# Kernel tuning notes

Hardware: AMD Instinct MI355X
Metric: run time of the kernel (lower is better)

The kernel has to match this reference:

```python
import jax, jax.numpy as jnp
import numpy as np

B, SQ, SK, H, HEADS, E, DFF = 4, 512, 1024, 1024, 16, 8, 4096
DH = H // HEADS
EPS = 1e-6


def _ln(x, g, b):
    m = jnp.mean(x, -1, keepdims=True)
    v = jnp.mean((x - m) ** 2, -1, keepdims=True)
    return (x - m) * jax.lax.rsqrt(v + EPS) * g + b


def setup_inputs() -> dict:
    key = jax.random.key(0)
    ks = jax.random.split(key, 16)
    s = 0.02
    return {
        "concated_input": jax.random.normal(ks[0], (B, SK, H), jnp.float32),
        "gen_emb": jax.random.normal(ks[1], (B, SQ, H), jnp.float32),
        "mask": jnp.zeros((B, 1, SQ, SK), jnp.float32),
        "ln_g": jnp.ones((H,), jnp.float32),
        "ln_b": jnp.zeros((H,), jnp.float32),
        "wq": jax.random.normal(ks[2], (H, H), jnp.float32) * s,
        "bq": jnp.zeros((H,), jnp.float32),
        "wk": jax.random.normal(ks[3], (H, H), jnp.float32) * s,
        "bk": jnp.zeros((H,), jnp.float32),
        "wv": jax.random.normal(ks[4], (H, H), jnp.float32) * s,
        "bv": jnp.zeros((H,), jnp.float32),
        "wo": jax.random.normal(ks[5], (H, H), jnp.float32) * s,
        "bo": jnp.zeros((H,), jnp.float32),
        "gw": jax.random.normal(ks[6], (H, E), jnp.float32) * s,
        "gb": jnp.zeros((E,), jnp.float32),
        "w1": jax.random.normal(ks[7], (E, H, DFF), jnp.float32) * s,
        "b1": jnp.zeros((E, DFF), jnp.float32),
        "w2": jax.random.normal(ks[8], (E, DFF, H), jnp.float32) * s,
        "b2": jnp.zeros((E, H), jnp.float32),
    }


def reference(concated_input, gen_emb, mask, ln_g, ln_b, wq, bq, wk, bk, wv, bv,
              wo, bo, gw, gb, w1, b1, w2, b2):
    residual_gen = gen_emb
    ctx_ln = _ln(concated_input, ln_g, ln_b)
    gen_ln = _ln(gen_emb, ln_g, ln_b)

    # multi-head cross attention: gen queries, concated keys/values
    q = (gen_ln @ wq + bq).reshape(B, SQ, HEADS, DH).transpose(0, 2, 1, 3)
    k = (ctx_ln @ wk + bk).reshape(B, SK, HEADS, DH).transpose(0, 2, 1, 3)
    v = (ctx_ln @ wv + bv).reshape(B, SK, HEADS, DH).transpose(0, 2, 1, 3)
    scores = jnp.einsum("bhqd,bhkd->bhqk", q, k) / np.sqrt(DH).astype(np.float32)
    attn = jax.nn.softmax(scores + mask, axis=-1)
    ctx_v = jnp.einsum("bhqk,bhkd->bhqd", attn, v)
    ctx_v = ctx_v.transpose(0, 2, 1, 3).reshape(B, SQ, H)
    ca_out = ctx_v @ wo + bo + residual_gen

    ln_ca = _ln(ca_out, ln_g, ln_b)

    # top-1 router on ca_out (pre-LN, as in original)
    gate = jax.nn.softmax(ca_out @ gw + gb, axis=-1)
    top_idx = jnp.argmax(gate, axis=-1)  # [B,SQ]

    # dense all-expert FFN, then gather selected expert (faithful to original)
    h1 = jax.nn.gelu(jnp.einsum("bsh,ehf->bsef", ln_ca, w1) + b1, approximate=False)
    expert_out = jnp.einsum("bsef,efh->bseh", h1, w2) + b2  # [B,SQ,E,H]
    sel = jnp.take_along_axis(expert_out, top_idx[:, :, None, None], axis=2)
    moe_out = sel[:, :, 0, :] + ln_ca
    return moe_out
```

## Files before the change

### kernel.cpp

```cpp
#include <hip/hip_runtime.h>
#include <stdint.h>
#include <stddef.h>

typedef _Float16 f16;
typedef _Float16 half8 __attribute__((ext_vector_type(8)));
typedef float f32x4 __attribute__((ext_vector_type(4)));

constexpr int kB = 4, kSQ = 512, kSK = 1024, kH = 1024, kHeads = 16, kE = 8, kDFF = 4096;
constexpr int kTok = kB * kSQ;

__device__ __forceinline__ void g2l16(const f16* g, f16* l) {
  __builtin_amdgcn_global_load_lds((const __attribute__((address_space(1))) uint32_t*)g,
                                   (__attribute__((address_space(3))) uint32_t*)l, 16, 0, 0);
}

__device__ __forceinline__ int xcd_swz(int phys, int nwg) {
  return (phys & 7) * (nwg >> 3) + (phys >> 3);
}

__global__ __launch_bounds__(256) void tr_f2h(const float* __restrict__ src,
                                              f16* __restrict__ dst, int R, int C) {
  __shared__ float t[32][33];
  long zo = (long)blockIdx.z * R * C;
  int r0 = blockIdx.y * 32, c0 = blockIdx.x * 32;
  int tr = threadIdx.x >> 3, tc = (threadIdx.x & 7) << 2;
  float4 v = *(const float4*)(src + zo + (long)(r0 + tr) * C + c0 + tc);
  t[tr][tc] = v.x; t[tr][tc + 1] = v.y; t[tr][tc + 2] = v.z; t[tr][tc + 3] = v.w;
  __syncthreads();
  union { f16 h[4]; uint2 u; } o;
  o.h[0] = (f16)t[tc + 0][tr]; o.h[1] = (f16)t[tc + 1][tr];
  o.h[2] = (f16)t[tc + 2][tr]; o.h[3] = (f16)t[tc + 3][tr];
  *(uint2*)(dst + zo + (long)(c0 + tr) * R + r0 + tc) = o.u;
}

struct Tr4P { const float* s0; const float* s1; const float* s2; const float* s3;
              f16* d0; f16* d1; f16* d2; f16* d3; };
__global__ __launch_bounds__(256) void tr_f2h4(Tr4P tp) {
  __shared__ float t[32][33];
  int z = blockIdx.z;
  const float* src = z == 0 ? tp.s0 : z == 1 ? tp.s1 : z == 2 ? tp.s2 : tp.s3;
  f16* dst = z == 0 ? tp.d0 : z == 1 ? tp.d1 : z == 2 ? tp.d2 : tp.d3;
  int r0 = blockIdx.y * 32, c0 = blockIdx.x * 32;
  int tr = threadIdx.x >> 3, tc = (threadIdx.x & 7) << 2;
  float4 v = *(const float4*)(src + (long)(r0 + tr) * kH + c0 + tc);
  t[tr][tc] = v.x; t[tr][tc + 1] = v.y; t[tr][tc + 2] = v.z; t[tr][tc + 3] = v.w;
  __syncthreads();
  union { f16 h[4]; uint2 u; } o;
  o.h[0] = (f16)t[tc + 0][tr]; o.h[1] = (f16)t[tc + 1][tr];
  o.h[2] = (f16)t[tc + 2][tr]; o.h[3] = (f16)t[tc + 3][tr];
  *(uint2*)(dst + (long)(c0 + tr) * kH + r0 + tc) = o.u;
}

__global__ __launch_bounds__(256) void ln_kernel(const float* __restrict__ x,
                                                 const float* __restrict__ g,
                                                 const float* __restrict__ b,
                                                 f16* __restrict__ oh, float* __restrict__ of,
                                                 int rows) {
  int row = blockIdx.x;
  if (row >= rows) return;
  int tid = threadIdx.x;
  const float* xr = x + (long)row * kH;
  float4 v = *(const float4*)(xr + tid * 4);
  float s = v.x + v.y + v.z + v.w;
  float s2 = v.x * v.x + v.y * v.y + v.z * v.z + v.w * v.w;
  __shared__ float red[8];
  for (int o = 32; o; o >>= 1) { s += __shfl_down(s, o); s2 += __shfl_down(s2, o); }
  int wv = tid >> 6, lane = tid & 63;
  if (lane == 0) { red[wv] = s; red[4 + wv] = s2; }
  __syncthreads();
  if (tid == 0) {
    red[0] = red[0] + red[1] + red[2] + red[3];
    red[4] = red[4] + red[5] + red[6] + red[7];
  }
  __syncthreads();
  float mean = red[0] * (1.0f / kH);
  float var = red[4] * (1.0f / kH) - mean * mean;
  float rs = rsqrtf(var + 1e-6f);
  float4 gv = *(const float4*)(g + tid * 4);
  float4 bv = *(const float4*)(b + tid * 4);
  float y0 = (v.x - mean) * rs * gv.x + bv.x;
  float y1 = (v.y - mean) * rs * gv.y + bv.y;
  float y2 = (v.z - mean) * rs * gv.z + bv.z;
  float y3 = (v.w - mean) * rs * gv.w + bv.w;
  long base = (long)row * kH + tid * 4;
  if (oh) {
    union { f16 h[4]; uint2 u; } o;
    o.h[0] = (f16)y0; o.h[1] = (f16)y1; o.h[2] = (f16)y2; o.h[3] = (f16)y3;
    *(uint2*)(oh + base) = o.u;
  }
  if (of) { float4 o4 = {y0, y1, y2, y3}; *(float4*)(of + base) = o4; }
}

__global__ void zero_kernel(int* __restrict__ p, int n) {
  int i = blockIdx.x * blockDim.x + threadIdx.x;
  if (i < n) p[i] = 0;
}

__global__ __launch_bounds__(64) void router_kernel(const float* __restrict__ ca,
                                                    const float* __restrict__ gw,
                                                    const float* __restrict__ gb,
                                                    int* __restrict__ cursors,
                                                    int* __restrict__ list,
                                                    int* __restrict__ eid) {
  int t = blockIdx.x;
  int lane = threadIdx.x;
  const float* x = ca + (long)t * kH;
  float acc[kE];
#pragma unroll
  for (int e = 0; e < kE; e++) acc[e] = 0.0f;
  for (int h = lane; h < kH; h += 64) {
    float xv = x[h];
    const float* gr = gw + (long)h * kE;
#pragma unroll
    for (int e = 0; e < kE; e++) acc[e] += xv * gr[e];
  }
#pragma unroll
  for (int e = 0; e < kE; e++)
    for (int o = 32; o; o >>= 1) acc[e] += __shfl_down(acc[e], o);
  if (lane == 0) {
    int best = 0;
    float bv = acc[0] + gb[0];
    for (int e = 1; e < kE; e++) {
      float v = acc[e] + gb[e];
      if (v > bv) { bv = v; best = e; }
    }
    int slot = atomicAdd(&cursors[best], 1);
    list[best * kTok + slot] = t;
    eid[t] = best;
  }
}

__global__ __launch_bounds__(256) void ffn2_reduce(const float* __restrict__ part,
                                                   const float* __restrict__ lnca,
                                                   const float* __restrict__ b2,
                                                   const int* __restrict__ eid,
                                                   float* __restrict__ out) {
  int t = blockIdx.x;
  int i = threadIdx.x * 4;
  int e = eid[t];
  long idx = (long)t * kH + i;
  float4 p0 = *(const float4*)(part + idx);
  float4 p1 = *(const float4*)(part + (long)kTok * kH + idx);
  float4 p2 = *(const float4*)(part + 2L * kTok * kH + idx);
  float4 p3 = *(const float4*)(part + 3L * kTok * kH + idx);
  float4 r  = *(const float4*)(lnca + idx);
  float4 bb = *(const float4*)(b2 + (long)e * kH + i);
  float4 o = {p0.x + p1.x + p2.x + p3.x + r.x + bb.x,
              p0.y + p1.y + p2.y + p3.y + r.y + bb.y,
              p0.z + p1.z + p2.z + p3.z + r.z + bb.z,
              p0.w + p1.w + p2.w + p3.w + r.w + bb.w};
  *(float4*)(out + idx) = o;
}

__global__ __launch_bounds__(256) void flash_kernel(const f16* __restrict__ q,
                                                    const f16* __restrict__ k,
                                                    const f16* __restrict__ v_t,
                                                    const float* __restrict__ mask,
                                                    f16* __restrict__ ctx) {
  __shared__ f16 Ks[64 * 64];
  __shared__ f16 Vs[64 * 64];
  __shared__ f16 Ps[4][16][72];
  int l = xcd_swz(blockIdx.x, gridDim.x);
  int qt = l & 7;
  int bh = l >> 3;
  int b = bh >> 4;
  int ho = (bh & 15) * 64;
  int tid = threadIdx.x, lane = tid & 63, wave = tid >> 6;
  int quad = lane >> 4, lo = lane & 15;

  long qg = ((long)b * kSQ + qt * 64 + wave * 16 + lo) * kH + ho;
  half8 aq0 = *(const half8*)(q + qg + quad * 8);
  half8 aq1 = *(const half8*)(q + qg + 32 + quad * 8);

  int srow = tid >> 3;
  int soct = (tid & 7) ^ (srow & 7);
  const f16* ksrc[2];
  const f16* vsrc[2];
#pragma unroll
  for (int s = 0; s < 2; s++) {
    int r = s * 32 + srow;
    ksrc[s] = k + ((long)b * kSK + r) * kH + ho + soct * 8;
    vsrc[s] = v_t + ((long)bh * 64 + r) * kSK + soct * 8;
  }
  const float* maskp = mask + ((long)b * kSQ + qt * 64 + wave * 16 + quad * 4) * kSK;

  float m_s[4] = {-1e30f, -1e30f, -1e30f, -1e30f};
  float l_s[4] = {0.f, 0.f, 0.f, 0.f};
  f32x4 O[4] = {};

  for (int kt = 0; kt < kSK / 64; kt++) {
    int sk0 = kt * 64;
#pragma unroll
    for (int s = 0; s < 2; s++) g2l16(ksrc[s] + (long)sk0 * kH, &Ks[(s * 256 + tid) * 8]);
#pragma unroll
    for (int s = 0; s < 2; s++) g2l16(vsrc[s] + sk0, &Vs[(s * 256 + tid) * 8]);
    __syncthreads();
    f32x4 sf[4] = {};
#pragma unroll
    for (int nt = 0; nt < 4; nt++) {
      int key = nt * 16 + lo;
      half8 bk0 = *(const half8*)&Ks[key * 64 + (((0 * 4 + quad)) ^ (key & 7)) * 8];
      half8 bk1 = *(const half8*)&Ks[key * 64 + (((1 * 4 + quad)) ^ (key & 7)) * 8];
      sf[nt] = __builtin_amdgcn_mfma_f32_16x16x32_f16(aq0, bk0, sf[nt], 0, 0, 0);
      sf[nt] = __builtin_amdgcn_mfma_f32_16x16x32_f16(aq1, bk1, sf[nt], 0, 0, 0);
    }
#pragma unroll
    for (int r = 0; r < 4; r++)
#pragma unroll
      for (int nt = 0; nt < 4; nt++)
        sf[nt][r] += maskp[(long)r * kSK + sk0 + nt * 16 + lo];
#pragma unroll
    for (int r = 0; r < 4; r++) {
      float mx = fmaxf(fmaxf(sf[0][r], sf[1][r]), fmaxf(sf[2][r], sf[3][r]));
      mx = fmaxf(mx, __shfl_xor(mx, 1));
      mx = fmaxf(mx, __shfl_xor(mx, 2));
      mx = fmaxf(mx, __shfl_xor(mx, 4));
      mx = fmaxf(mx, __shfl_xor(mx, 8));
      float m_new = fmaxf(m_s[r], mx);
      float alpha = __expf(m_s[r] - m_new);
      m_s[r] = m_new;
      float p0 = __expf(sf[0][r] - m_new), p1 = __expf(sf[1][r] - m_new);
      float p2 = __expf(sf[2][r] - m_new), p3 = __expf(sf[3][r] - m_new);
      float rs = p0 + p1 + p2 + p3;
      rs += __shfl_xor(rs, 1);
      rs += __shfl_xor(rs, 2);
      rs += __shfl_xor(rs, 4);
      rs += __shfl_xor(rs, 8);
      l_s[r] = l_s[r] * alpha + rs;
#pragma unroll
      for (int nt = 0; nt < 4; nt++) O[nt][r] *= alpha;
      Ps[wave][quad * 4 + r][0 * 16 + lo] = (f16)p0;
      Ps[wave][quad * 4 + r][1 * 16 + lo] = (f16)p1;
      Ps[wave][quad * 4 + r][2 * 16 + lo] = (f16)p2;
      Ps[wave][quad * 4 + r][3 * 16 + lo] = (f16)p3;
    }
    half8 ap0 = *(const half8*)&Ps[wave][lo][quad * 8];
    half8 ap1 = *(const half8*)&Ps[wave][lo][32 + quad * 8];
#pragma unroll
    for (int nt = 0; nt < 4; nt++) {
      int d = nt * 16 + lo;
      half8 bv0 = *(const half8*)&Vs[d * 64 + (((0 * 4 + quad)) ^ (d & 7)) * 8];
      half8 bv1 = *(const half8*)&Vs[d * 64 + (((1 * 4 + quad)) ^ (d & 7)) * 8];
      O[nt] = __builtin_amdgcn_mfma_f32_16x16x32_f16(ap0, bv0, O[nt], 0, 0, 0);
      O[nt] = __builtin_amdgcn_mfma_f32_16x16x32_f16(ap1, bv1, O[nt], 0, 0, 0);
    }
    __syncthreads();
  }
#pragma unroll
  for (int r = 0; r < 4; r++) {
    float inv = 1.0f / l_s[r];
    long row = (long)b * kSQ + qt * 64 + wave * 16 + quad * 4 + r;
#pragma unroll
    for (int nt = 0; nt < 4; nt++)
      ctx[row * kH + ho + nt * 16 + lo] = (f16)(O[nt][r] * inv);
  }
}

struct GemmP {
  const f16* A; long a_row, a_z1, a_z2;
  const f16* Bm; long b_nstr, b_z1, b_z2;
  float* Cf; f16* Ch; long c_row, c_z1, c_z2, c_split; int c_tr;
  const float* bias; long bias_z;
  const float* res; long res_row, res_z1, res_z2;
  float alpha; int gelu; int ksplit;
  int M, N, K, zdiv;
  int gx, gy;
  const int* glist; const int* cnt;
};

template <int BM, int BN>
__device__ __forceinline__ void gemm_body(const GemmP& p, int bx, int by, int bz,
                                          f16* A0, f16* A1, f16* B0, f16* B1) {
  constexpr int FM = BM / 32, FN = BN / 64;
  constexpr int SA = BM / 64, SB = BN / 64;
  int z = bz;
  int kb = 0, kEnd = p.K, ks = 0;
  if (p.ksplit > 1) {
    int kc = p.K / p.ksplit;
    ks = z % p.ksplit;
    kb = ks * kc;
    kEnd = kb + kc;
    z /= p.ksplit;
  }
  long aoff = 0, boff = 0, coff = 0, roff = 0, biasoff = 0;
  const int* gl = nullptr;
  int Meff = p.M;
  if (p.glist) {
    Meff = p.cnt[z];
    gl = p.glist + (long)z * kTok;
    boff = (long)z * p.b_z2;
    biasoff = (long)z * p.bias_z;
  } else {
    int z1 = z / p.zdiv, z2 = z % p.zdiv;
    aoff = (long)z1 * p.a_z1 + (long)z2 * p.a_z2;
    boff = (long)z1 * p.b_z1 + (long)z2 * p.b_z2;
    coff = (long)z1 * p.c_z1 + (long)z2 * p.c_z2;
    roff = (long)z1 * p.res_z1 + (long)z2 * p.res_z2;
  }
  coff += (long)ks * p.c_split;
  int m0 = by * BM;
  if (m0 >= Meff) return;
  int n0 = bx * BN;
  int tid = threadIdx.x, lane = tid & 63, wave = tid >> 6;
  int wm = (wave & 1) * (BM / 2), wn = (wave >> 1) * (BN / 4);
  int q = lane >> 4, lo = lane & 15;

  int srow = tid >> 3;
  int soct = (tid & 7) ^ (srow & 7);
  const f16* asrc[SA];
  const f16* bsrc[SB];
#pragma unroll
  for (int s = 0; s < SA; s++) {
    int row = m0 + s * 64 + srow;
    if (gl) row = gl[row < Meff ? row : Meff - 1];
    asrc[s] = p.A + aoff + (long)row * p.a_row + soct * 8;
  }
#pragma unroll
  for (int s = 0; s < SB; s++)
    bsrc[s] = p.Bm + boff + (long)(n0 + s * 64 + srow) * p.b_nstr + soct * 8;

  f32x4 acc[FM][FN] = {};

  auto stage = [&](f16* Ad, f16* Bd, int k0) {
#pragma unroll
    for (int s = 0; s < SA; s++) g2l16(asrc[s] + k0, &Ad[(s * 512 + tid) * 8]);
#pragma unroll
    for (int s = 0; s < SB; s++) g2l16(bsrc[s] + k0, &Bd[(s * 512 + tid) * 8]);
  };
  auto compute = [&](const f16* As, const f16* Bs) {
    half8 af[2][FM], bf[2][FN];
#pragma unroll
    for (int kk = 0; kk < 2; kk++) {
#pragma unroll
      for (int i = 0; i < FM; i++) {
        int r = wm + i * 16 + lo;
        af[kk][i] = *(const half8*)&As[r * 64 + ((kk * 4 + q) ^ (r & 7)) * 8];
      }
#pragma unroll
      for (int j = 0; j < FN; j++) {
        int n = wn + j * 16 + lo;
        bf[kk][j] = *(const half8*)&Bs[n * 64 + ((kk * 4 + q) ^ (n & 7)) * 8];
      }
    }
#pragma unroll
    for (int kk = 0; kk < 2; kk++)
#pragma unroll
      for (int i = 0; i < FM; i++)
#pragma unroll
        for (int j = 0; j < FN; j++)
          acc[i][j] = __builtin_amdgcn_mfma_f32_16x16x32_f16(af[kk][i], bf[kk][j], acc[i][j], 0, 0, 0);
  };

  stage(A0, B0, kb);
  __syncthreads();
  for (int k0 = kb; k0 < kEnd; k0 += 128) {
    if (k0 + 64 < kEnd) stage(A1, B1, k0 + 64);
    compute(A0, B0);
    __syncthreads();
    if (k0 + 64 < kEnd) {
      if (k0 + 128 < kEnd) stage(A0, B0, k0 + 128);
      compute(A1, B1);
      __syncthreads();
    }
  }

#pragma unroll
  for (int i = 0; i < FM; i++) {
#pragma unroll
    for (int j = 0; j < FN; j++) {
      int col = n0 + wn + j * 16 + lo;
      if (p.c_tr) {
        int row0 = m0 + wm + i * 16 + q * 4;
        union { f16 h[4]; uint2 u; } o;
#pragma unroll
        for (int r = 0; r < 4; r++) {
          float v = acc[i][j][r];
          if (p.bias) v += p.bias[biasoff + col];
          v *= p.alpha;
          o.h[r] = (f16)v;
        }
        *(uint2*)&p.Ch[coff + (long)col * p.c_row + row0] = o.u;
      } else {
#pragma unroll
        for (int r = 0; r < 4; r++) {
          int row = m0 + wm + i * 16 + q * 4 + r;
          if (row < Meff) {
            long rr = gl ? (long)gl[row] : (long)row;
            float v = acc[i][j][r];
            if (p.bias) v += p.bias[biasoff + col];
            v *= p.alpha;
            if (p.res) v += p.res[roff + rr * p.res_row + col];
            if (p.gelu) v = 0.5f * v * (1.0f + erff(v * 0.70710678118654752f));
            long ci = coff + rr * p.c_row + col;
            if (p.Cf) p.Cf[ci] = v;
            else p.Ch[ci] = (f16)v;
          }
        }
      }
    }
  }
}

template <int BM, int BN>
__global__ __launch_bounds__(512) void gemm_t(GemmP p) {
  __shared__ f16 A0[BM * 64], A1[BM * 64], B0[BN * 64], B1[BN * 64];
  int l = xcd_swz(blockIdx.x, gridDim.x);
  int bx = l % p.gx;
  int r = l / p.gx;
  int by = r % p.gy;
  int bz = r / p.gy;
  gemm_body<BM, BN>(p, bx, by, bz, A0, A1, B0, B1);
}

struct Multi3P {
  GemmP g0, g1, g2;
  int n0, n1;
  int gx0, gy0, gx1, gy1, gx2, gy2;
};

__global__ __launch_bounds__(512) void gemm_qkv(Multi3P mp) {
  __shared__ f16 A0[128 * 64], A1[128 * 64], B0[128 * 64], B1[128 * 64];
  int fb = xcd_swz(blockIdx.x, gridDim.x);
  if (fb < mp.n0) {
    gemm_body<128, 128>(mp.g0, fb % mp.gx0, (fb / mp.gx0) % mp.gy0, fb / (mp.gx0 * mp.gy0),
                        A0, A1, B0, B1);
    return;
  }
  fb -= mp.n0;
  if (fb < mp.n1) {
    gemm_body<128, 128>(mp.g1, fb % mp.gx1, (fb / mp.gx1) % mp.gy1, fb / (mp.gx1 * mp.gy1),
                        A0, A1, B0, B1);
    return;
  }
  fb -= mp.n1;
  gemm_body<128, 128>(mp.g2, fb % mp.gx2, (fb / mp.gx2) % mp.gy2, fb / (mp.gx2 * mp.gy2),
                      A0, A1, B0, B1);
}

extern "C" void kernel_launch(void* const* d_in, const int* in_sizes, int n_in,
                              void* d_out, int out_size, void* d_ws, size_t ws_size,
                              hipStream_t stream) {
  const float* concated = (const float*)d_in[0];
  const float* gen      = (const float*)d_in[1];
  const float* mask     = (const float*)d_in[2];
  const float* ln_g     = (const float*)d_in[3];
  const float* ln_b     = (const float*)d_in[4];
  const float* wq = (const float*)d_in[5];  const float* bq = (const float*)d_in[6];
  const float* wk = (const float*)d_in[7];  const float* bk = (const float*)d_in[8];
  const float* wv = (const float*)d_in[9];  const float* bv = (const float*)d_in[10];
  const float* wo = (const float*)d_in[11]; const float* bo = (const float*)d_in[12];
  const float* gw = (const float*)d_in[13]; const float* gb = (const float*)d_in[14];
  const float* w1 = (const float*)d_in[15]; const float* b1 = (const float*)d_in[16];
  const float* w2 = (const float*)d_in[17]; const float* b2 = (const float*)d_in[18];
  float* out = (float*)d_out;

  size_t off = 0;
  auto alloc = [&](size_t bytes) -> void* {
    void* p = (char*)d_ws + off;
    off += (bytes + 255) & ~(size_t)255;
    return p;
  };
  f16* wq_t  = (f16*)alloc((size_t)kH * kH * 2);
  f16* wk_t  = (f16*)alloc((size_t)kH * kH * 2);
  f16* wv_t  = (f16*)alloc((size_t)kH * kH * 2);
  f16* wo_t  = (f16*)alloc((size_t)kH * kH * 2);
  f16* w1_t  = (f16*)alloc((size_t)kE * kH * kDFF * 2);
  f16* w2_t  = (f16*)alloc((size_t)kE * kDFF * kH * 2);
  f16* lnc_h = (f16*)alloc((size_t)kB * kSK * kH * 2);
  f16* lng_h = (f16*)alloc((size_t)kTok * kH * 2);
  f16* q_h   = (f16*)alloc((size_t)kTok * kH * 2);
  f16* k_h   = (f16*)alloc((size_t)kB * kSK * kH * 2);
  f16* v_t   = (f16*)alloc((size_t)kB * kSK * kH * 2);
  f16* ctx_h = (f16*)alloc((size_t)kTok * kH * 2);
  float* ca_f   = (float*)alloc((size_t)kTok * kH * 4);
  float* lnca_f = (float*)alloc((size_t)kTok * kH * 4);
  f16* lnca_h   = (f16*)alloc((size_t)kTok * kH * 2);
  f16* h1_h     = (f16*)alloc((size_t)kTok * kDFF * 2);
  float* part_f = (float*)alloc((size_t)4 * kTok * kH * 4);
  int* cnt_d    = (int*)alloc(kE * 4);
  int* list_d   = (int*)alloc((size_t)kE * kTok * 4);
  int* eid_d    = (int*)alloc((size_t)kTok * 4);

  {
    Tr4P tp{wq, wk, wv, wo, wq_t, wk_t, wv_t, wo_t};
    tr_f2h4<<<dim3(32, 32, 4), 256, 0, stream>>>(tp);
  }
  tr_f2h<<<dim3(kDFF / 32, kH / 32, kE), 256, 0, stream>>>(w1, w1_t, kH, kDFF);
  tr_f2h<<<dim3(kH / 32, kDFF / 32, kE), 256, 0, stream>>>(w2, w2_t, kDFF, kH);

  ln_kernel<<<kB * kSK, 256, 0, stream>>>(concated, ln_g, ln_b, lnc_h, nullptr, kB * kSK);
  ln_kernel<<<kTok, 256, 0, stream>>>(gen, ln_g, ln_b, lng_h, nullptr, kTok);

  {
    Multi3P mp{};
    GemmP& pq = mp.g0;
    pq.A = lng_h; pq.a_row = kH; pq.Bm = wq_t; pq.b_nstr = kH;
    pq.Ch = q_h; pq.c_row = kH; pq.bias = bq; pq.alpha = 0.125f;
    pq.M = kTok; pq.N = kH; pq.K = kH; pq.zdiv = 1;
    GemmP& pk = mp.g1;
    pk.A = lnc_h; pk.a_row = kH; pk.Bm = wk_t; pk.b_nstr = kH;
    pk.Ch = k_h; pk.c_row = kH; pk.bias = bk; pk.alpha = 1.0f;
    pk.M = kB * kSK; pk.N = kH; pk.K = kH; pk.zdiv = 1;
    GemmP& pv = mp.g2;
    pv.A = lnc_h; pv.a_row = kH; pv.a_z1 = (long)kSK * kH;
    pv.Bm = wv_t; pv.b_nstr = kH;
    pv.Ch = v_t; pv.c_row = kSK; pv.c_z1 = (long)kH * kSK; pv.c_tr = 1;
    pv.bias = bv; pv.alpha = 1.0f;
    pv.M = kSK; pv.N = kH; pv.K = kH; pv.zdiv = 1;
    mp.gx0 = kH / 128; mp.gy0 = kTok / 128;        mp.n0 = mp.gx0 * mp.gy0;
    mp.gx1 = kH / 128; mp.gy1 = (kB * kSK) / 128;  mp.n1 = mp.gx1 * mp.gy1;
    mp.gx2 = kH / 128; mp.gy2 = kSK / 128;
    int ntot = mp.n0 + mp.n1 + mp.gx2 * mp.gy2 * kB;
    gemm_qkv<<<dim3(ntot), 512, 0, stream>>>(mp);
  }
  flash_kernel<<<dim3((kSQ / 64) * kB * kHeads), 256, 0, stream>>>(q_h, k_h, v_t, mask, ctx_h);
  {
    GemmP p{}; p.A = ctx_h; p.a_row = kH;
    p.Bm = wo_t; p.b_nstr = kH;
    p.Cf = ca_f; p.c_row = kH; p.bias = bo;
    p.res = gen; p.res_row = kH;
    p.alpha = 1.0f; p.M = kTok; p.N = kH; p.K = kH; p.zdiv = 1;
    p.gx = kH / 64; p.gy = kTok / 64;
    gemm_t<64, 64><<<dim3(p.gx * p.gy), 512, 0, stream>>>(p);
  }
  ln_kernel<<<kTok, 256, 0, stream>>>(ca_f, ln_g, ln_b, lnca_h, lnca_f, kTok);
  zero_kernel<<<1, 64, 0, stream>>>(cnt_d, kE);
  router_kernel<<<kTok, 64, 0, stream>>>(ca_f, gw, gb, cnt_d, list_d, eid_d);
  {
    GemmP p{}; p.A = lnca_h; p.a_row = kH;
    p.Bm = w1_t; p.b_nstr = kH; p.b_z2 = (long)kH * kDFF;
    p.Ch = h1_h; p.c_row = kDFF; p.bias = b1; p.bias_z = kDFF;
    p.alpha = 1.0f; p.gelu = 1; p.M = kTok; p.N = kDFF; p.K = kH; p.zdiv = 1;
    p.glist = list_d; p.cnt = cnt_d;
    p.gx = kDFF / 128; p.gy = kTok / 128;
    gemm_t<128, 128><<<dim3(p.gx * p.gy * kE), 512, 0, stream>>>(p);
  }
  {
    GemmP p{}; p.A = h1_h; p.a_row = kDFF;
    p.Bm = w2_t; p.b_nstr = kDFF; p.b_z2 = (long)kDFF * kH;
    p.Cf = part_f; p.c_row = kH; p.c_split = (long)kTok * kH;
    p.alpha = 1.0f; p.ksplit = 4;
    p.M = kTok; p.N = kH; p.K = kDFF; p.zdiv = 1;
    p.glist = list_d; p.cnt = cnt_d;
    p.gx = kH / 128; p.gy = kTok / 128;
    gemm_t<128, 128><<<dim3(p.gx * p.gy * kE * 4), 512, 0, stream>>>(p);
  }
  ffn2_reduce<<<kTok, 256, 0, stream>>>(part_f, lnca_f, b2, eid_d, out);
}
```

Baseline: 625.1 us.

## Double-buffer flash K/V tiles and merge small prep kernel launches

Flash attention now double-buffers its K/V tiles in LDS, issuing the next tile's async global-to-LDS loads before computing the current tile, so memory latency can overlap MFMA work. The two w1/w2 transpose launches are merged into one grid, the two input layernorms into one kernel, and the counter-zeroing kernel is folded into the post-attention layernorm. Together these cut launch count and exposed load latency, at the cost of doubled K/V LDS use in flash, which may lower occupancy.

```diff
diff --git a/kernel.cpp b/kernel.cpp
--- a/kernel.cpp
+++ b/kernel.cpp
@@ -16,21 +16,6 @@
 
 __device__ __forceinline__ int xcd_swz(int phys, int nwg) {
   return (phys & 7) * (nwg >> 3) + (phys >> 3);
-}
-
-__global__ __launch_bounds__(256) void tr_f2h(const float* __restrict__ src,
-                                              f16* __restrict__ dst, int R, int C) {
-  __shared__ float t[32][33];
-  long zo = (long)blockIdx.z * R * C;
-  int r0 = blockIdx.y * 32, c0 = blockIdx.x * 32;
-  int tr = threadIdx.x >> 3, tc = (threadIdx.x & 7) << 2;
-  float4 v = *(const float4*)(src + zo + (long)(r0 + tr) * C + c0 + tc);
-  t[tr][tc] = v.x; t[tr][tc + 1] = v.y; t[tr][tc + 2] = v.z; t[tr][tc + 3] = v.w;
-  __syncthreads();
-  union { f16 h[4]; uint2 u; } o;
-  o.h[0] = (f16)t[tc + 0][tr]; o.h[1] = (f16)t[tc + 1][tr];
-  o.h[2] = (f16)t[tc + 2][tr]; o.h[3] = (f16)t[tc + 3][tr];
-  *(uint2*)(dst + zo + (long)(c0 + tr) * R + r0 + tc) = o.u;
 }
 
 struct Tr4P { const float* s0; const float* s1; const float* s2; const float* s3;
@@ -51,14 +36,81 @@
   *(uint2*)(dst + (long)(c0 + tr) * kH + r0 + tc) = o.u;
 }
 
+__global__ __launch_bounds__(256) void tr_f2h_w12(const float* __restrict__ w1,
+                                                  const float* __restrict__ w2,
+                                                  f16* __restrict__ w1_t,
+                                                  f16* __restrict__ w2_t) {
+  __shared__ float t[32][33];
+  int z = blockIdx.z;
+  const float* src;
+  f16* dst;
+  int R, C, cx, ry;
+  if (z < 8) {
+    src = w1 + (long)z * kH * kDFF; dst = w1_t + (long)z * kH * kDFF;
+    R = kH; C = kDFF; cx = blockIdx.x; ry = blockIdx.y;
+  } else {
+    src = w2 + (long)(z - 8) * kDFF * kH; dst = w2_t + (long)(z - 8) * kDFF * kH;
+    R = kDFF; C = kH;
+    int ft = blockIdx.y * 128 + blockIdx.x;
+    cx = ft & 31; ry = ft >> 5;
+  }
+  int r0 = ry * 32, c0 = cx * 32;
+  int tr = threadIdx.x >> 3, tc = (threadIdx.x & 7) << 2;
+  float4 v = *(const float4*)(src + (long)(r0 + tr) * C + c0 + tc);
+  t[tr][tc] = v.x; t[tr][tc + 1] = v.y; t[tr][tc + 2] = v.z; t[tr][tc + 3] = v.w;
+  __syncthreads();
+  union { f16 h[4]; uint2 u; } o;
+  o.h[0] = (f16)t[tc + 0][tr]; o.h[1] = (f16)t[tc + 1][tr];
+  o.h[2] = (f16)t[tc + 2][tr]; o.h[3] = (f16)t[tc + 3][tr];
+  *(uint2*)(dst + (long)(c0 + tr) * R + r0 + tc) = o.u;
+}
+
+__global__ __launch_bounds__(256) void ln2_kernel(const float* __restrict__ x0,
+                                                  const float* __restrict__ x1,
+                                                  const float* __restrict__ g,
+                                                  const float* __restrict__ b,
+                                                  f16* __restrict__ o0,
+                                                  f16* __restrict__ o1, int rows0) {
+  int row = blockIdx.x;
+  const float* xr;
+  f16* orow;
+  if (row < rows0) { xr = x0 + (long)row * kH; orow = o0 + (long)row * kH; }
+  else { int r2 = row - rows0; xr = x1 + (long)r2 * kH; orow = o1 + (long)r2 * kH; }
+  int tid = threadIdx.x;
+  float4 v = *(const float4*)(xr + tid * 4);
+  float s = v.x + v.y + v.z + v.w;
+  float s2 = v.x * v.x + v.y * v.y + v.z * v.z + v.w * v.w;
+  __shared__ float red[8];
+  for (int o = 32; o; o >>= 1) { s += __shfl_down(s, o); s2 += __shfl_down(s2, o); }
+  int wv = tid >> 6, lane = tid & 63;
+  if (lane == 0) { red[wv] = s; red[4 + wv] = s2; }
+  __syncthreads();
+  if (tid == 0) {
+    red[0] = red[0] + red[1] + red[2] + red[3];
+    red[4] = red[4] + red[5] + red[6] + red[7];
+  }
+  __syncthreads();
+  float mean = red[0] * (1.0f / kH);
+  float var = red[4] * (1.0f / kH) - mean * mean;
+  float rs = rsqrtf(var + 1e-6f);
+  float4 gv = *(const float4*)(g + tid * 4);
+  float4 bv = *(const float4*)(b + tid * 4);
+  union { f16 h[4]; uint2 u; } o;
+  o.h[0] = (f16)((v.x - mean) * rs * gv.x + bv.x);
+  o.h[1] = (f16)((v.y - mean) * rs * gv.y + bv.y);
+  o.h[2] = (f16)((v.z - mean) * rs * gv.z + bv.z);
+  o.h[3] = (f16)((v.w - mean) * rs * gv.w + bv.w);
+  *(uint2*)(orow + tid * 4) = o.u;
+}
+
 __global__ __launch_bounds__(256) void ln_kernel(const float* __restrict__ x,
                                                  const float* __restrict__ g,
                                                  const float* __restrict__ b,
                                                  f16* __restrict__ oh, float* __restrict__ of,
-                                                 int rows) {
+                                                 int* __restrict__ zc) {
   int row = blockIdx.x;
-  if (row >= rows) return;
   int tid = threadIdx.x;
+  if (zc && row == 0 && tid < kE) zc[tid] = 0;
   const float* xr = x + (long)row * kH;
   float4 v = *(const float4*)(xr + tid * 4);
   float s = v.x + v.y + v.z + v.w;
@@ -83,17 +135,11 @@
   float y2 = (v.z - mean) * rs * gv.z + bv.z;
   float y3 = (v.w - mean) * rs * gv.w + bv.w;
   long base = (long)row * kH + tid * 4;
-  if (oh) {
-    union { f16 h[4]; uint2 u; } o;
-    o.h[0] = (f16)y0; o.h[1] = (f16)y1; o.h[2] = (f16)y2; o.h[3] = (f16)y3;
-    *(uint2*)(oh + base) = o.u;
-  }
-  if (of) { float4 o4 = {y0, y1, y2, y3}; *(float4*)(of + base) = o4; }
-}
-
-__global__ void zero_kernel(int* __restrict__ p, int n) {
-  int i = blockIdx.x * blockDim.x + threadIdx.x;
-  if (i < n) p[i] = 0;
+  union { f16 h[4]; uint2 u; } o;
+  o.h[0] = (f16)y0; o.h[1] = (f16)y1; o.h[2] = (f16)y2; o.h[3] = (f16)y3;
+  *(uint2*)(oh + base) = o.u;
+  float4 o4 = {y0, y1, y2, y3};
+  *(float4*)(of + base) = o4;
 }
 
 __global__ __launch_bounds__(64) void router_kernel(const float* __restrict__ ca,
@@ -157,8 +203,8 @@
                                                     const f16* __restrict__ v_t,
                                                     const float* __restrict__ mask,
                                                     f16* __restrict__ ctx) {
-  __shared__ f16 Ks[64 * 64];
-  __shared__ f16 Vs[64 * 64];
+  __shared__ f16 Ks0[64 * 64], Ks1[64 * 64];
+  __shared__ f16 Vs0[64 * 64], Vs1[64 * 64];
   __shared__ f16 Ps[4][16][72];
   int l = xcd_swz(blockIdx.x, gridDim.x);
   int qt = l & 7;
@@ -188,19 +234,20 @@
   float l_s[4] = {0.f, 0.f, 0.f, 0.f};
   f32x4 O[4] = {};
 
-  for (int kt = 0; kt < kSK / 64; kt++) {
+  auto stageKV = [&](f16* Kd, f16* Vd, int sk0) {
+#pragma unroll
+    for (int s = 0; s < 2; s++) g2l16(ksrc[s] + (long)sk0 * kH, &Kd[(s * 256 + tid) * 8]);
+#pragma unroll
+    for (int s = 0; s < 2; s++) g2l16(vsrc[s] + sk0, &Vd[(s * 256 + tid) * 8]);
+  };
+  auto computeT = [&](const f16* Kc, const f16* Vc, int kt) {
     int sk0 = kt * 64;
-#pragma unroll
-    for (int s = 0; s < 2; s++) g2l16(ksrc[s] + (long)sk0 * kH, &Ks[(s * 256 + tid) * 8]);
-#pragma unroll
-    for (int s = 0; s < 2; s++) g2l16(vsrc[s] + sk0, &Vs[(s * 256 + tid) * 8]);
-    __syncthreads();
     f32x4 sf[4] = {};
 #pragma unroll
     for (int nt = 0; nt < 4; nt++) {
       int key = nt * 16 + lo;
-      half8 bk0 = *(const half8*)&Ks[key * 64 + (((0 * 4 + quad)) ^ (key & 7)) * 8];
-      half8 bk1 = *(const half8*)&Ks[key * 64 + (((1 * 4 + quad)) ^ (key & 7)) * 8];
+      half8 bk0 = *(const half8*)&Kc[key * 64 + (((0 * 4 + quad)) ^ (key & 7)) * 8];
+      half8 bk1 = *(const half8*)&Kc[key * 64 + (((1 * 4 + quad)) ^ (key & 7)) * 8];
       sf[nt] = __builtin_amdgcn_mfma_f32_16x16x32_f16(aq0, bk0, sf[nt], 0, 0, 0);
       sf[nt] = __builtin_amdgcn_mfma_f32_16x16x32_f16(aq1, bk1, sf[nt], 0, 0, 0);
     }
@@ -239,12 +286,25 @@
 #pragma unroll
     for (int nt = 0; nt < 4; nt++) {
       int d = nt * 16 + lo;
-      half8 bv0 = *(const half8*)&Vs[d * 64 + (((0 * 4 + quad)) ^ (d & 7)) * 8];
-      half8 bv1 = *(const half8*)&Vs[d * 64 + (((1 * 4 + quad)) ^ (d & 7)) * 8];
+      half8 bv0 = *(const half8*)&Vc[d * 64 + (((0 * 4 + quad)) ^ (d & 7)) * 8];
+      half8 bv1 = *(const half8*)&Vc[d * 64 + (((1 * 4 + quad)) ^ (d & 7)) * 8];
       O[nt] = __builtin_amdgcn_mfma_f32_16x16x32_f16(ap0, bv0, O[nt], 0, 0, 0);
       O[nt] = __builtin_amdgcn_mfma_f32_16x16x32_f16(ap1, bv1, O[nt], 0, 0, 0);
     }
+  };
+
+  constexpr int NT = kSK / 64;
+  stageKV(Ks0, Vs0, 0);
+  __syncthreads();
+  for (int kt = 0; kt < NT; kt += 2) {
+    if (kt + 1 < NT) stageKV(Ks1, Vs1, (kt + 1) * 64);
+    computeT(Ks0, Vs0, kt);
     __syncthreads();
+    if (kt + 1 < NT) {
+      if (kt + 2 < NT) stageKV(Ks0, Vs0, (kt + 2) * 64);
+      computeT(Ks1, Vs1, kt + 1);
+      __syncthreads();
+    }
   }
 #pragma unroll
   for (int r = 0; r < 4; r++) {
@@ -485,11 +545,10 @@
     Tr4P tp{wq, wk, wv, wo, wq_t, wk_t, wv_t, wo_t};
     tr_f2h4<<<dim3(32, 32, 4), 256, 0, stream>>>(tp);
   }
-  tr_f2h<<<dim3(kDFF / 32, kH / 32, kE), 256, 0, stream>>>(w1, w1_t, kH, kDFF);
-  tr_f2h<<<dim3(kH / 32, kDFF / 32, kE), 256, 0, stream>>>(w2, w2_t, kDFF, kH);
-
-  ln_kernel<<<kB * kSK, 256, 0, stream>>>(concated, ln_g, ln_b, lnc_h, nullptr, kB * kSK);
-  ln_kernel<<<kTok, 256, 0, stream>>>(gen, ln_g, ln_b, lng_h, nullptr, kTok);
+  tr_f2h_w12<<<dim3(128, 32, 16), 256, 0, stream>>>(w1, w2, w1_t, w2_t);
+
+  ln2_kernel<<<kB * kSK + kTok, 256, 0, stream>>>(concated, gen, ln_g, ln_b,
+                                                  lnc_h, lng_h, kB * kSK);
 
   {
     Multi3P mp{};
@@ -523,8 +582,7 @@
     p.gx = kH / 64; p.gy = kTok / 64;
     gemm_t<64, 64><<<dim3(p.gx * p.gy), 512, 0, stream>>>(p);
   }
-  ln_kernel<<<kTok, 256, 0, stream>>>(ca_f, ln_g, ln_b, lnca_h, lnca_f, kTok);
-  zero_kernel<<<1, 64, 0, stream>>>(cnt_d, kE);
+  ln_kernel<<<kTok, 256, 0, stream>>>(ca_f, ln_g, ln_b, lnca_h, lnca_f, cnt_d);
   router_kernel<<<kTok, 64, 0, stream>>>(ca_f, gw, gb, cnt_d, list_d, eid_d);
   {
     GemmP p{}; p.A = lnca_h; p.a_row = kH;
```

Result: no change. 621.4 us (-0.6%).
